# Kernel tuning notes

Hardware: AMD Instinct MI355X
Metric: run time of the kernel (lower is better)

## Reference

```python
import jax, jax.numpy as jnp
import numpy as np

B, S, D, H, DH = 2, 2048, 768, 12, 64
ROT, BASE, WIN = 64, 10000.0, 128
SCALE = float(np.sqrt(DH))  # cfg.attn_scale = sqrt(d_head) = 8.0


def _sin_cos():
    # TransformerLens calculate_sin_cos_rotary, rotary_adjacent_pairs=False
    pos = jnp.arange(S, dtype=jnp.float32)
    freq = BASE ** (jnp.arange(0, ROT, 2, dtype=jnp.float32) / ROT)
    freq = jnp.concatenate([freq, freq])  # 'd -> (2 d)'
    angles = pos[:, None] / freq[None, :]  # [S, ROT]
    return jnp.sin(angles), jnp.cos(angles)


def _rotate_every_two(v):
    n = v.shape[-1] // 2
    return jnp.concatenate([-v[..., n:], v[..., :n]], axis=-1)


def _apply_rotary(x, sin, cos):
    # x: [B, S, H, DH]; rotate first ROT dims, pass rest through
    xr, xp = x[..., :ROT], x[..., ROT:]
    c = cos[None, :, None, :]
    s = sin[None, :, None, :]
    return jnp.concatenate([xr * c + _rotate_every_two(xr) * s, xp], axis=-1)


def setup_inputs() -> dict:
    key = jax.random.key(0)
    ks = jax.random.split(key, 7)
    init = lambda k, shape: jax.random.normal(k, shape, jnp.float32) / np.sqrt(D).astype(np.float32)
    return dict(
        query_input=jax.random.normal(ks[0], (B, S, D), jnp.float32),
        key_input=jax.random.normal(ks[1], (B, S, D), jnp.float32),
        value_input=jax.random.normal(ks[2], (B, S, D), jnp.float32),
        W_Q=init(ks[3], (H, D, DH)),
        W_K=init(ks[4], (H, D, DH)),
        W_V=init(ks[5], (H, D, DH)),
        W_O=init(ks[6], (H, DH, D)),
        b_Q=jnp.zeros((H, DH), jnp.float32),
        b_K=jnp.zeros((H, DH), jnp.float32),
        b_V=jnp.zeros((H, DH), jnp.float32),
        b_O=jnp.zeros((D,), jnp.float32),
    )


def reference(query_input, key_input, value_input, W_Q, W_K, W_V, W_O, b_Q, b_K, b_V, b_O):
    # QKV projections (calculate_qkv_matrices)
    q = jnp.einsum('bpd,hdk->bphk', query_input, W_Q) + b_Q
    k = jnp.einsum('bpd,hdk->bphk', key_input, W_K) + b_K
    v = jnp.einsum('bpd,hdk->bphk', value_input, W_V) + b_V
    # rotary (kv_cache_pos_offset = 0)
    sin, cos = _sin_cos()
    q = _apply_rotary(q, sin, cos)
    k = _apply_rotary(k, sin, cos)
    # attention scores
    scores = jnp.einsum('bqhd,bkhd->bhqk', q, k) / SCALE
    # position_bias defaults to zeros -> no-op
    i = jnp.arange(S)[:, None]
    j = jnp.arange(S)[None, :]
    mask = (j <= i) & (j > i - WIN)
    scores = jnp.where(mask[None, None], scores, -jnp.inf)
    pattern = jax.nn.softmax(scores, axis=-1)
    pattern = jnp.where(jnp.isnan(pattern), 0.0, pattern)
    z = jnp.einsum('bhqk,bkhd->bqhd', pattern, v)  # [B, S, H, DH]
    # output projection: z flattened @ W_O (rearranged) + b_O
    out = z.reshape(B, S, H * DH) @ W_O.reshape(H * DH, D) + b_O
    return out
```

## Files before the change

### kernel.cpp

```cpp
#include <hip/hip_runtime.h>
#include <hip/hip_bf16.h>

#define BB 2
#define SS 2048
#define DD 768
#define HH 12
#define DHH 64
#define WIN 128
#define MM (BB*SS)

typedef __attribute__((ext_vector_type(8))) short bfrag;
typedef __attribute__((ext_vector_type(4))) float f32x4;

#define AS3(p) ((__attribute__((address_space(3))) void*)(p))
#define AS1(p) ((const __attribute__((address_space(1))) void*)(p))

__device__ inline unsigned short f2bf(float f) {
    union { __hip_bfloat16 h; unsigned short u; } cv;
    cv.h = __float2bfloat16(f);
    return cv.u;
}

__device__ inline void stage128(unsigned short* dst, const unsigned short* src,
                                int w4, int l) {
    #pragma unroll
    for (int j = 0; j < 2; j++) {
        int eoff = (w4 * 2 + j) * 512;
        int e = eoff + l * 8;
        int row = e >> 5;
        int k8 = ((e >> 3) & 3) ^ ((row >> 1) & 3);
        __builtin_amdgcn_global_load_lds(AS1(src + (size_t)row * DD + k8 * 8),
                                         AS3(dst + eoff), 16, 0, 0);
    }
}
__device__ inline void stage64(unsigned short* dst, const unsigned short* src,
                               int w4, int l) {
    int eoff = w4 * 512;
    int e = eoff + l * 8;
    int row = e >> 5;
    int k8 = ((e >> 3) & 3) ^ ((row >> 1) & 3);
    __builtin_amdgcn_global_load_lds(AS1(src + (size_t)row * DD + k8 * 8),
                                     AS3(dst + eoff), 16, 0, 0);
}

__global__ __launch_bounds__(256) void pack_kernel(
    const float* __restrict__ Xq, const float* __restrict__ Xk, const float* __restrict__ Xv,
    const float* __restrict__ Wq, const float* __restrict__ Wk, const float* __restrict__ Wv,
    const float* __restrict__ Wo,
    unsigned short* __restrict__ Wt, unsigned short* __restrict__ Wot,
    float2* __restrict__ rope, unsigned short* __restrict__ Xbf)
{
    __shared__ float T[64][65];
    const int bid = blockIdx.x, t = threadIdx.x;
    if (bid < 432) {
        int proj = bid / 144, rem = bid % 144;
        int h = rem / 12, d0 = (rem % 12) * 64;
        const float* src = (proj == 0 ? Wq : (proj == 1 ? Wk : Wv)) + (size_t)h * DD * DHH;
        int row = t >> 2, c0 = (t & 3) * 16;
        const float4* p4 = reinterpret_cast<const float4*>(src + (size_t)(d0 + row) * DHH + c0);
        float4 x0 = p4[0], x1 = p4[1], x2 = p4[2], x3 = p4[3];
        float* tr = &T[row][c0];
        tr[0]=x0.x; tr[1]=x0.y; tr[2]=x0.z; tr[3]=x0.w;
        tr[4]=x1.x; tr[5]=x1.y; tr[6]=x1.z; tr[7]=x1.w;
        tr[8]=x2.x; tr[9]=x2.y; tr[10]=x2.z; tr[11]=x2.w;
        tr[12]=x3.x; tr[13]=x3.y; tr[14]=x3.z; tr[15]=x3.w;
        __syncthreads();
        int dh = t >> 2;
        unsigned short tmp[16];
        #pragma unroll
        for (int j = 0; j < 16; j++) tmp[j] = f2bf(T[c0 + j][dh]);
        unsigned short* dst = Wt + (size_t)proj * DD * DD + (size_t)(h * 64 + dh) * DD + d0 + c0;
        *reinterpret_cast<bfrag*>(dst)     = *reinterpret_cast<bfrag*>(tmp);
        *reinterpret_cast<bfrag*>(dst + 8) = *reinterpret_cast<bfrag*>(tmp + 8);
    } else if (bid < 576) {
        int id2 = bid - 432;
        int k0 = (id2 / 12) * 64, n0 = (id2 % 12) * 64;
        int row = t >> 2, c0 = (t & 3) * 16;
        const float4* p4 = reinterpret_cast<const float4*>(Wo + (size_t)(k0 + row) * DD + n0 + c0);
        float4 x0 = p4[0], x1 = p4[1], x2 = p4[2], x3 = p4[3];
        float* tr = &T[row][c0];
        tr[0]=x0.x; tr[1]=x0.y; tr[2]=x0.z; tr[3]=x0.w;
        tr[4]=x1.x; tr[5]=x1.y; tr[6]=x1.z; tr[7]=x1.w;
        tr[8]=x2.x; tr[9]=x2.y; tr[10]=x2.z; tr[11]=x2.w;
        tr[12]=x3.x; tr[13]=x3.y; tr[14]=x3.z; tr[15]=x3.w;
        __syncthreads();
        int nr = t >> 2;
        unsigned short tmp[16];
        #pragma unroll
        for (int j = 0; j < 16; j++) tmp[j] = f2bf(T[c0 + j][nr]);
        unsigned short* dst = Wot + (size_t)(n0 + nr) * DD + k0 + c0;
        *reinterpret_cast<bfrag*>(dst)     = *reinterpret_cast<bfrag*>(tmp);
        *reinterpret_cast<bfrag*>(dst + 8) = *reinterpret_cast<bfrag*>(tmp + 8);
    } else if (bid < 832) {
        int idx = (bid - 576) * 256 + t;
        int p = idx >> 5, i2 = idx & 31;
        float inv_freq = exp2f(-(float)i2 * (13.287712379549449f / 32.0f));
        float s, c;
        sincosf((float)p * inv_freq, &s, &c);
        rope[idx] = make_float2(s, c);
    } else {
        int i = bid - 832;
        int proj = i / 768;
        size_t off = (size_t)(i % 768) * 4096 + t * 16;
        const float* src = (proj == 0 ? Xq : (proj == 1 ? Xk : Xv)) + off;
        const float4* p4 = reinterpret_cast<const float4*>(src);
        float4 a0 = p4[0], a1 = p4[1], a2 = p4[2], a3 = p4[3];
        unsigned short u[16];
        u[0]=f2bf(a0.x); u[1]=f2bf(a0.y); u[2]=f2bf(a0.z); u[3]=f2bf(a0.w);
        u[4]=f2bf(a1.x); u[5]=f2bf(a1.y); u[6]=f2bf(a1.z); u[7]=f2bf(a1.w);
        u[8]=f2bf(a2.x); u[9]=f2bf(a2.y); u[10]=f2bf(a2.z); u[11]=f2bf(a2.w);
        u[12]=f2bf(a3.x); u[13]=f2bf(a3.y); u[14]=f2bf(a3.z); u[15]=f2bf(a3.w);
        unsigned short* dst = Xbf + (size_t)proj * MM * DD + off;
        *reinterpret_cast<bfrag*>(dst)     = *reinterpret_cast<bfrag*>(u);
        *reinterpret_cast<bfrag*>(dst + 8) = *reinterpret_cast<bfrag*>(u + 8);
    }
}

__global__ __launch_bounds__(256) void qkv_gemm_kernel(
    const unsigned short* __restrict__ Xbf,
    const unsigned short* __restrict__ Wt,
    const float* __restrict__ bq, const float* __restrict__ bk, const float* __restrict__ bv,
    const float2* __restrict__ rope,
    unsigned short* __restrict__ qo, unsigned short* __restrict__ ko, unsigned short* __restrict__ vo)
{
    const int mt0  = blockIdx.x * 128;
    const int n0   = blockIdx.y * 128;
    const int proj = blockIdx.z;
    const unsigned short* X = Xbf + (size_t)proj * MM * DD + (size_t)mt0 * DD;
    const unsigned short* W = Wt + (size_t)proj * DD * DD + (size_t)n0 * DD;
    const float* bias = proj == 0 ? bq : (proj == 1 ? bk : bv);

    __shared__ unsigned short smem[128 * 140];

    const int t = threadIdx.x;
    const int l = t & 63, w4 = t >> 6;
    const int l16 = l & 15, quad = l >> 4;
    const int wr = w4 >> 1, wc = w4 & 1;
    const int swz = (l16 >> 1) & 3;

    f32x4 acc[16] = {};

    stage128(smem,        X, w4, l);
    stage128(smem + 4096, W, w4, l);

    for (int it = 0; it < 24; ++it) {
        unsigned short* Ac = smem + (it & 1) * 8192;
        unsigned short* Bc = Ac + 4096;
        __syncthreads();
        if (it < 23) {
            unsigned short* An = smem + ((it + 1) & 1) * 8192;
            stage128(An,        X + (it + 1) * 32, w4, l);
            stage128(An + 4096, W + (it + 1) * 32, w4, l);
        }
        bfrag af[4], bg[4];
        #pragma unroll
        for (int mi = 0; mi < 4; mi++)
            af[mi] = *reinterpret_cast<const bfrag*>(&Ac[(wr * 64 + mi * 16 + l16) * 32 + ((quad ^ swz) * 8)]);
        #pragma unroll
        for (int ni = 0; ni < 4; ni++)
            bg[ni] = *reinterpret_cast<const bfrag*>(&Bc[(wc * 64 + ni * 16 + l16) * 32 + ((quad ^ swz) * 8)]);
        #pragma unroll
        for (int mi = 0; mi < 4; mi++)
            #pragma unroll
            for (int ni = 0; ni < 4; ni++)
                acc[mi * 4 + ni] = __builtin_amdgcn_mfma_f32_16x16x32_bf16(af[mi], bg[ni], acc[mi * 4 + ni], 0, 0, 0);
    }
    __syncthreads();

    unsigned short* Ct = smem;
    const int b = mt0 >> 11;
    if (proj < 2) {
        #pragma unroll
        for (int ni = 0; ni < 4; ni++) {
            int nloc = wc * 64 + ni * 16 + l16;
            int n = n0 + nloc;
            int dh = n & 63;
            float bv0 = bias[n];
            float bv1 = bias[n ^ 32];
            float sgn = (dh & 32) ? 1.0f : -1.0f;
            const float2* rp = rope + (dh & 31);
            #pragma unroll
            for (int mi = 0; mi < 4; mi++)
                #pragma unroll
                for (int r = 0; r < 4; r++) {
                    int ploc = wr * 64 + mi * 16 + quad * 4 + r;
                    int p = (mt0 + ploc) & (SS - 1);
                    float2 sc = rp[p << 5];
                    float val = acc[mi * 4 + ni][r] + bv0;
                    float pr  = acc[mi * 4 + (ni ^ 2)][r] + bv1;
                    Ct[ploc * 140 + nloc] = f2bf(val * sc.y + sgn * pr * sc.x);
                }
        }
        __syncthreads();
        unsigned short* dst = (proj == 0) ? qo : ko;
        #pragma unroll
        for (int jj = 0; jj < 8; jj++) {
            int id = jj * 256 + t;
            int row = id >> 4, c = (id & 15) * 8;
            int n = n0 + c, h = n >> 6, dh = n & 63;
            int p = (mt0 + row) & (SS - 1);
            bfrag vv = *reinterpret_cast<const bfrag*>(&Ct[row * 140 + c]);
            *reinterpret_cast<bfrag*>(dst + (((size_t)(b * HH + h) * SS + p) << 6) + dh) = vv;
        }
    } else {
        #pragma unroll
        for (int ni = 0; ni < 4; ni++) {
            int nloc = wc * 64 + ni * 16 + l16;
            float bv0 = bias[n0 + nloc];
            #pragma unroll
            for (int mi = 0; mi < 4; mi++)
                #pragma unroll
                for (int r = 0; r < 4; r++) {
                    int ploc = wr * 64 + mi * 16 + quad * 4 + r;
                    Ct[nloc * 140 + ploc] = f2bf(acc[mi * 4 + ni][r] + bv0);
                }
        }
        __syncthreads();
        int p0 = mt0 & (SS - 1);
        #pragma unroll
        for (int jj = 0; jj < 8; jj++) {
            int id = jj * 256 + t;
            int row = id >> 4, c = (id & 15) * 8;
            int n = n0 + row, h = n >> 6, dh = n & 63;
            bfrag vv = *reinterpret_cast<const bfrag*>(&Ct[row * 140 + c]);
            *reinterpret_cast<bfrag*>(vo + (((size_t)(b * HH + h) * DHH + dh) << 11) + p0 + c) = vv;
        }
    }
}

__global__ __launch_bounds__(256) void attn_kernel(
    const unsigned short* __restrict__ q,
    const unsigned short* __restrict__ k,
    const unsigned short* __restrict__ v,
    unsigned short* __restrict__ z)
{
    const int qb = blockIdx.x * 64;
    const int h  = blockIdx.y;
    const int b  = blockIdx.z;
    const int kb = qb - WIN;

    __shared__ unsigned short QK[64 * 72 + 192 * 72];
    __shared__ unsigned short Ps[64 * 200];
    unsigned short* Qs = QK;
    unsigned short* Ks = QK + 64 * 72;
    unsigned short* Vt = QK;

    const int t = threadIdx.x;
    const int w = t >> 6, lane = t & 63;
    const int l16 = lane & 15, quad = lane >> 4;

    const size_t qkbase = ((size_t)(b * HH + h) * SS) * DHH;
    #pragma unroll
    for (int i = 0; i < 2; i++) {
        int chunk = i * 256 + t;
        int row = chunk >> 3, c0 = (chunk & 7) * 8;
        bfrag val = *reinterpret_cast<const bfrag*>(q + qkbase + (size_t)(qb + row) * DHH + c0);
        *reinterpret_cast<bfrag*>(&Qs[row * 72 + c0]) = val;
    }
    #pragma unroll
    for (int i = 0; i < 6; i++) {
        int chunk = i * 256 + t;
        int row = chunk >> 3, c0 = (chunk & 7) * 8;
        int src = kb + row; if (src < 0) src = 0;
        bfrag val = *reinterpret_cast<const bfrag*>(k + qkbase + (size_t)src * DHH + c0);
        *reinterpret_cast<bfrag*>(&Ks[row * 72 + c0]) = val;
    }
    __syncthreads();

    f32x4 sacc[12] = {};
    #pragma unroll
    for (int kk = 0; kk < 64; kk += 32) {
        bfrag a = *reinterpret_cast<const bfrag*>(&Qs[(16 * w + l16) * 72 + kk + quad * 8]);
        #pragma unroll
        for (int mt = 0; mt < 12; mt++) {
            bfrag bf = *reinterpret_cast<const bfrag*>(&Ks[(16 * mt + l16) * 72 + kk + quad * 8]);
            sacc[mt] = __builtin_amdgcn_mfma_f32_16x16x32_bf16(a, bf, sacc[mt], 0, 0, 0);
        }
    }

    float mx[4] = {-3e38f, -3e38f, -3e38f, -3e38f};
    #pragma unroll
    for (int mt = 0; mt < 12; mt++)
        #pragma unroll
        for (int r = 0; r < 4; r++) {
            int row = 16 * w + quad * 4 + r;
            int c = 16 * mt + l16;
            bool valid = (c > row) && (c <= row + WIN) && (kb + c >= 0);
            float s = valid ? sacc[mt][r] * 0.125f : -3e38f;
            sacc[mt][r] = s;
            mx[r] = fmaxf(mx[r], s);
        }
    #pragma unroll
    for (int off = 1; off < 16; off <<= 1)
        #pragma unroll
        for (int r = 0; r < 4; r++) mx[r] = fmaxf(mx[r], __shfl_xor(mx[r], off, 64));
    float sum[4] = {0.f, 0.f, 0.f, 0.f};
    #pragma unroll
    for (int mt = 0; mt < 12; mt++)
        #pragma unroll
        for (int r = 0; r < 4; r++) {
            float p = __expf(sacc[mt][r] - mx[r]);
            sacc[mt][r] = p;
            sum[r] += p;
        }
    #pragma unroll
    for (int off = 1; off < 16; off <<= 1)
        #pragma unroll
        for (int r = 0; r < 4; r++) sum[r] += __shfl_xor(sum[r], off, 64);
    float inv[4];
    #pragma unroll
    for (int r = 0; r < 4; r++) inv[r] = 1.0f / sum[r];

    #pragma unroll
    for (int mt = 0; mt < 12; mt++)
        #pragma unroll
        for (int r = 0; r < 4; r++)
            Ps[(16 * w + quad * 4 + r) * 200 + 16 * mt + l16] = f2bf(sacc[mt][r] * inv[r]);
    __syncthreads();

    const size_t vbase = ((size_t)(b * HH + h) * DHH) * SS;
    if (kb >= 0) {
        #pragma unroll
        for (int i = 0; i < 6; i++) {
            int chunk = i * 256 + t;
            int d = chunk / 24, c0 = (chunk % 24) * 8;
            bfrag val = *reinterpret_cast<const bfrag*>(v + vbase + (size_t)d * SS + kb + c0);
            *reinterpret_cast<bfrag*>(&Vt[d * 200 + c0]) = val;
        }
    } else {
        for (int i = 0; i < 6; i++) {
            int chunk = i * 256 + t;
            int d = chunk / 24, c0 = (chunk % 24) * 8;
            unsigned short tmp[8];
            for (int j2 = 0; j2 < 8; j2++) {
                int src = kb + c0 + j2; if (src < 0) src = 0;
                tmp[j2] = v[vbase + (size_t)d * SS + src];
            }
            for (int j2 = 0; j2 < 8; j2++) Vt[d * 200 + c0 + j2] = tmp[j2];
        }
    }
    __syncthreads();

    f32x4 zacc[4] = {};
    #pragma unroll
    for (int c0 = 0; c0 < 192; c0 += 32) {
        bfrag a = *reinterpret_cast<const bfrag*>(&Ps[(16 * w + l16) * 200 + c0 + quad * 8]);
        #pragma unroll
        for (int nt = 0; nt < 4; nt++) {
            bfrag bf = *reinterpret_cast<const bfrag*>(&Vt[(16 * nt + l16) * 200 + c0 + quad * 8]);
            zacc[nt] = __builtin_amdgcn_mfma_f32_16x16x32_bf16(a, bf, zacc[nt], 0, 0, 0);
        }
    }
    #pragma unroll
    for (int nt = 0; nt < 4; nt++)
        #pragma unroll
        for (int r = 0; r < 4; r++) {
            int row = 16 * w + quad * 4 + r;
            int d = 16 * nt + l16;
            z[((size_t)(b * SS + qb + row)) * (HH * DHH) + h * DHH + d] = f2bf(zacc[nt][r]);
        }
}

__global__ __launch_bounds__(256) void out_gemm_kernel(
    const unsigned short* __restrict__ Z,
    const unsigned short* __restrict__ Wot,
    const float* __restrict__ bo,
    float* __restrict__ out)
{
    const int mt0 = blockIdx.x * 64;
    const int n0  = blockIdx.y * 128;
    const unsigned short* A = Z + (size_t)mt0 * DD;
    const unsigned short* Bw = Wot + (size_t)n0 * DD;

    __shared__ unsigned short smem[12288];

    const int t = threadIdx.x;
    const int l = t & 63, w4 = t >> 6;
    const int l16 = l & 15, quad = l >> 4;
    const int swz = (l16 >> 1) & 3;

    f32x4 acc[8] = {};

    stage64 (smem,        A,  w4, l);
    stage128(smem + 2048, Bw, w4, l);

    for (int it = 0; it < 24; ++it) {
        unsigned short* Ac = smem + (it & 1) * 6144;
        unsigned short* Bc = Ac + 2048;
        __syncthreads();
        if (it < 23) {
            unsigned short* An = smem + ((it + 1) & 1) * 6144;
            stage64 (An,        A  + (it + 1) * 32, w4, l);
            stage128(An + 2048, Bw + (it + 1) * 32, w4, l);
        }
        bfrag af[4], bg[2];
        #pragma unroll
        for (int mi = 0; mi < 4; mi++)
            af[mi] = *reinterpret_cast<const bfrag*>(&Ac[(mi * 16 + l16) * 32 + ((quad ^ swz) * 8)]);
        #pragma unroll
        for (int ni = 0; ni < 2; ni++)
            bg[ni] = *reinterpret_cast<const bfrag*>(&Bc[(w4 * 32 + ni * 16 + l16) * 32 + ((quad ^ swz) * 8)]);
        #pragma unroll
        for (int mi = 0; mi < 4; mi++)
            #pragma unroll
            for (int ni = 0; ni < 2; ni++)
                acc[mi * 2 + ni] = __builtin_amdgcn_mfma_f32_16x16x32_bf16(af[mi], bg[ni], acc[mi * 2 + ni], 0, 0, 0);
    }

    #pragma unroll
    for (int ni = 0; ni < 2; ni++) {
        int n = n0 + w4 * 32 + ni * 16 + l16;
        float bv0 = bo[n];
        #pragma unroll
        for (int mi = 0; mi < 4; mi++)
            #pragma unroll
            for (int r = 0; r < 4; r++) {
                int m = mt0 + mi * 16 + quad * 4 + r;
                out[(size_t)m * DD + n] = acc[mi * 2 + ni][r] + bv0;
            }
    }
}

extern "C" void kernel_launch(void* const* d_in, const int* in_sizes, int n_in,
                              void* d_out, int out_size, void* d_ws, size_t ws_size,
                              hipStream_t stream) {
    const float* Xq = (const float*)d_in[0];
    const float* Xk = (const float*)d_in[1];
    const float* Xv = (const float*)d_in[2];
    const float* Wq = (const float*)d_in[3];
    const float* Wk = (const float*)d_in[4];
    const float* Wv = (const float*)d_in[5];
    const float* Wo = (const float*)d_in[6];
    const float* bq = (const float*)d_in[7];
    const float* bk = (const float*)d_in[8];
    const float* bv = (const float*)d_in[9];
    const float* bo = (const float*)d_in[10];
    float* out = (float*)d_out;

    const size_t seg = (size_t)BB * HH * SS * DHH;
    unsigned short* q   = (unsigned short*)d_ws;
    unsigned short* k   = q + seg;
    unsigned short* v   = k + seg;
    unsigned short* z   = v + seg;
    unsigned short* Wt  = z + seg;
    unsigned short* Wot = Wt + (size_t)3 * DD * DD;
    float2* rope = (float2*)(Wot + (size_t)DD * DD);
    unsigned short* Xbf = (unsigned short*)(rope + 2048 * 32);

    pack_kernel<<<dim3(3136), 256, 0, stream>>>(Xq, Xk, Xv, Wq, Wk, Wv, Wo, Wt, Wot, rope, Xbf);
    qkv_gemm_kernel<<<dim3(MM / 128, DD / 128, 3), 256, 0, stream>>>(
        Xbf, Wt, bq, bk, bv, rope, q, k, v);
    attn_kernel<<<dim3(SS / 64, HH, BB), 256, 0, stream>>>(q, k, v, z);
    out_gemm_kernel<<<dim3(MM / 64, DD / 128), 256, 0, stream>>>(z, Wot, bo, out);
}
```

Before: 169.1 us.

## Shrink QKV GEMM M-tile to 64 and restructure attention operand staging

The QKV GEMM moves from 128x128 to 64x128 tiles, doubling the grid and cutting shared memory so more blocks can be resident. The attention kernel now stages K into swizzled LDS with async global-to-LDS loads, keeps Q and V fragments in registers loaded straight from global memory, and reuses the K buffer for the probabilities. It computes Z transposed so each lane stores a 4-wide packed vector. This removes the separate V staging pass and one barrier, at the cost of more register pressure. For the first query block kb is negative, so the V and K loads read before the start of the buffer instead of clamping, and correctness there depends on masking alone.

```diff
diff --git a/kernel.cpp b/kernel.cpp
--- a/kernel.cpp
+++ b/kernel.cpp
@@ -11,6 +11,7 @@
 
 typedef __attribute__((ext_vector_type(8))) short bfrag;
 typedef __attribute__((ext_vector_type(4))) float f32x4;
+typedef __attribute__((ext_vector_type(4))) short s16x4;
 
 #define AS3(p) ((__attribute__((address_space(3))) void*)(p))
 #define AS1(p) ((const __attribute__((address_space(1))) void*)(p))
@@ -19,28 +20,6 @@
     union { __hip_bfloat16 h; unsigned short u; } cv;
     cv.h = __float2bfloat16(f);
     return cv.u;
-}
-
-__device__ inline void stage128(unsigned short* dst, const unsigned short* src,
-                                int w4, int l) {
-    #pragma unroll
-    for (int j = 0; j < 2; j++) {
-        int eoff = (w4 * 2 + j) * 512;
-        int e = eoff + l * 8;
-        int row = e >> 5;
-        int k8 = ((e >> 3) & 3) ^ ((row >> 1) & 3);
-        __builtin_amdgcn_global_load_lds(AS1(src + (size_t)row * DD + k8 * 8),
-                                         AS3(dst + eoff), 16, 0, 0);
-    }
-}
-__device__ inline void stage64(unsigned short* dst, const unsigned short* src,
-                               int w4, int l) {
-    int eoff = w4 * 512;
-    int e = eoff + l * 8;
-    int row = e >> 5;
-    int k8 = ((e >> 3) & 3) ^ ((row >> 1) & 3);
-    __builtin_amdgcn_global_load_lds(AS1(src + (size_t)row * DD + k8 * 8),
-                                     AS3(dst + eoff), 16, 0, 0);
 }
 
 __global__ __launch_bounds__(256) void pack_kernel(
@@ -123,14 +102,14 @@
     const float2* __restrict__ rope,
     unsigned short* __restrict__ qo, unsigned short* __restrict__ ko, unsigned short* __restrict__ vo)
 {
-    const int mt0  = blockIdx.x * 128;
+    const int mt0  = blockIdx.x * 64;
     const int n0   = blockIdx.y * 128;
     const int proj = blockIdx.z;
     const unsigned short* X = Xbf + (size_t)proj * MM * DD + (size_t)mt0 * DD;
     const unsigned short* W = Wt + (size_t)proj * DD * DD + (size_t)n0 * DD;
     const float* bias = proj == 0 ? bq : (proj == 1 ? bk : bv);
 
-    __shared__ unsigned short smem[128 * 140];
+    __shared__ unsigned short smem[12288];
 
     const int t = threadIdx.x;
     const int l = t & 63, w4 = t >> 6;
@@ -138,29 +117,48 @@
     const int wr = w4 >> 1, wc = w4 & 1;
     const int swz = (l16 >> 1) & 3;
 
-    f32x4 acc[16] = {};
-
-    stage128(smem,        X, w4, l);
-    stage128(smem + 4096, W, w4, l);
+    f32x4 acc[8] = {};
+
+    #define STAGE_QKV(bufp, k0)                                                   \
+        _Pragma("unroll")                                                         \
+        for (int j = 0; j < 3; j++) {                                             \
+            int g = w4 * 3 + j;                                                   \
+            if (g < 4) {                                                          \
+                int e = g * 512 + l * 8;                                          \
+                int row = e >> 5;                                                 \
+                int k8 = ((e >> 3) & 3) ^ ((row >> 1) & 3);                       \
+                __builtin_amdgcn_global_load_lds(                                 \
+                    AS1(X + (size_t)row * DD + (k0) + k8 * 8),                    \
+                    AS3((bufp) + g * 512), 16, 0, 0);                             \
+            } else {                                                              \
+                int g2 = g - 4;                                                   \
+                int e = g2 * 512 + l * 8;                                         \
+                int row = e >> 5;                                                 \
+                int k8 = ((e >> 3) & 3) ^ ((row >> 1) & 3);                       \
+                __builtin_amdgcn_global_load_lds(                                 \
+                    AS1(W + (size_t)row * DD + (k0) + k8 * 8),                    \
+                    AS3((bufp) + 2048 + g2 * 512), 16, 0, 0);                     \
+            }                                                                     \
+        }
+
+    STAGE_QKV(smem, 0)
 
     for (int it = 0; it < 24; ++it) {
-        unsigned short* Ac = smem + (it & 1) * 8192;
-        unsigned short* Bc = Ac + 4096;
+        unsigned short* cur = smem + (it & 1) * 6144;
         __syncthreads();
         if (it < 23) {
-            unsigned short* An = smem + ((it + 1) & 1) * 8192;
-            stage128(An,        X + (it + 1) * 32, w4, l);
-            stage128(An + 4096, W + (it + 1) * 32, w4, l);
-        }
-        bfrag af[4], bg[4];
-        #pragma unroll
-        for (int mi = 0; mi < 4; mi++)
-            af[mi] = *reinterpret_cast<const bfrag*>(&Ac[(wr * 64 + mi * 16 + l16) * 32 + ((quad ^ swz) * 8)]);
+            unsigned short* nxt = smem + ((it + 1) & 1) * 6144;
+            STAGE_QKV(nxt, (it + 1) * 32)
+        }
+        bfrag af[2], bg[4];
+        #pragma unroll
+        for (int mi = 0; mi < 2; mi++)
+            af[mi] = *reinterpret_cast<const bfrag*>(&cur[(wr * 32 + mi * 16 + l16) * 32 + ((quad ^ swz) * 8)]);
         #pragma unroll
         for (int ni = 0; ni < 4; ni++)
-            bg[ni] = *reinterpret_cast<const bfrag*>(&Bc[(wc * 64 + ni * 16 + l16) * 32 + ((quad ^ swz) * 8)]);
-        #pragma unroll
-        for (int mi = 0; mi < 4; mi++)
+            bg[ni] = *reinterpret_cast<const bfrag*>(&cur[2048 + (wc * 64 + ni * 16 + l16) * 32 + ((quad ^ swz) * 8)]);
+        #pragma unroll
+        for (int mi = 0; mi < 2; mi++)
             #pragma unroll
             for (int ni = 0; ni < 4; ni++)
                 acc[mi * 4 + ni] = __builtin_amdgcn_mfma_f32_16x16x32_bf16(af[mi], bg[ni], acc[mi * 4 + ni], 0, 0, 0);
@@ -169,6 +167,7 @@
 
     unsigned short* Ct = smem;
     const int b = mt0 >> 11;
+    const int p0 = mt0 & (SS - 1);
     if (proj < 2) {
         #pragma unroll
         for (int ni = 0; ni < 4; ni++) {
@@ -180,12 +179,11 @@
             float sgn = (dh & 32) ? 1.0f : -1.0f;
             const float2* rp = rope + (dh & 31);
             #pragma unroll
-            for (int mi = 0; mi < 4; mi++)
+            for (int mi = 0; mi < 2; mi++)
                 #pragma unroll
                 for (int r = 0; r < 4; r++) {
-                    int ploc = wr * 64 + mi * 16 + quad * 4 + r;
-                    int p = (mt0 + ploc) & (SS - 1);
-                    float2 sc = rp[p << 5];
+                    int ploc = wr * 32 + mi * 16 + quad * 4 + r;
+                    float2 sc = rp[(p0 + ploc) << 5];
                     float val = acc[mi * 4 + ni][r] + bv0;
                     float pr  = acc[mi * 4 + (ni ^ 2)][r] + bv1;
                     Ct[ploc * 140 + nloc] = f2bf(val * sc.y + sgn * pr * sc.x);
@@ -194,13 +192,12 @@
         __syncthreads();
         unsigned short* dst = (proj == 0) ? qo : ko;
         #pragma unroll
-        for (int jj = 0; jj < 8; jj++) {
+        for (int jj = 0; jj < 4; jj++) {
             int id = jj * 256 + t;
             int row = id >> 4, c = (id & 15) * 8;
             int n = n0 + c, h = n >> 6, dh = n & 63;
-            int p = (mt0 + row) & (SS - 1);
             bfrag vv = *reinterpret_cast<const bfrag*>(&Ct[row * 140 + c]);
-            *reinterpret_cast<bfrag*>(dst + (((size_t)(b * HH + h) * SS + p) << 6) + dh) = vv;
+            *reinterpret_cast<bfrag*>(dst + (((size_t)(b * HH + h) * SS + p0 + row) << 6) + dh) = vv;
         }
     } else {
         #pragma unroll
@@ -208,24 +205,24 @@
             int nloc = wc * 64 + ni * 16 + l16;
             float bv0 = bias[n0 + nloc];
             #pragma unroll
-            for (int mi = 0; mi < 4; mi++)
+            for (int mi = 0; mi < 2; mi++)
                 #pragma unroll
                 for (int r = 0; r < 4; r++) {
-                    int ploc = wr * 64 + mi * 16 + quad * 4 + r;
-                    Ct[nloc * 140 + ploc] = f2bf(acc[mi * 4 + ni][r] + bv0);
+                    int ploc = wr * 32 + mi * 16 + quad * 4 + r;
+                    Ct[nloc * 72 + ploc] = f2bf(acc[mi * 4 + ni][r] + bv0);
                 }
         }
         __syncthreads();
-        int p0 = mt0 & (SS - 1);
-        #pragma unroll
-        for (int jj = 0; jj < 8; jj++) {
+        #pragma unroll
+        for (int jj = 0; jj < 4; jj++) {
             int id = jj * 256 + t;
-            int row = id >> 4, c = (id & 15) * 8;
+            int row = id >> 3, c = (id & 7) * 8;
             int n = n0 + row, h = n >> 6, dh = n & 63;
-            bfrag vv = *reinterpret_cast<const bfrag*>(&Ct[row * 140 + c]);
+            bfrag vv = *reinterpret_cast<const bfrag*>(&Ct[row * 72 + c]);
             *reinterpret_cast<bfrag*>(vo + (((size_t)(b * HH + h) * DHH + dh) << 11) + p0 + c) = vv;
         }
     }
+    #undef STAGE_QKV
 }
 
 __global__ __launch_bounds__(256) void attn_kernel(
@@ -239,51 +236,69 @@
     const int b  = blockIdx.z;
     const int kb = qb - WIN;
 
-    __shared__ unsigned short QK[64 * 72 + 192 * 72];
-    __shared__ unsigned short Ps[64 * 200];
-    unsigned short* Qs = QK;
-    unsigned short* Ks = QK + 64 * 72;
-    unsigned short* Vt = QK;
+    __shared__ unsigned short sA[12800];
 
     const int t = threadIdx.x;
-    const int w = t >> 6, lane = t & 63;
-    const int l16 = lane & 15, quad = lane >> 4;
-
-    const size_t qkbase = ((size_t)(b * HH + h) * SS) * DHH;
-    #pragma unroll
-    for (int i = 0; i < 2; i++) {
-        int chunk = i * 256 + t;
-        int row = chunk >> 3, c0 = (chunk & 7) * 8;
-        bfrag val = *reinterpret_cast<const bfrag*>(q + qkbase + (size_t)(qb + row) * DHH + c0);
-        *reinterpret_cast<bfrag*>(&Qs[row * 72 + c0]) = val;
-    }
-    #pragma unroll
-    for (int i = 0; i < 6; i++) {
-        int chunk = i * 256 + t;
-        int row = chunk >> 3, c0 = (chunk & 7) * 8;
-        int src = kb + row; if (src < 0) src = 0;
-        bfrag val = *reinterpret_cast<const bfrag*>(k + qkbase + (size_t)src * DHH + c0);
-        *reinterpret_cast<bfrag*>(&Ks[row * 72 + c0]) = val;
-    }
+    const int w4 = t >> 6, l = t & 63;
+    const int l16 = l & 15, quad = l >> 4;
+    const int swz = (l16 >> 1) & 3;
+
+    const size_t qkbase = (size_t)(b * HH + h) * SS * DHH;
+    const unsigned short* kp = (k + qkbase) + (ptrdiff_t)kb * DHH;
+    const unsigned short* vp = (v + (size_t)(b * HH + h) * DHH * SS) + (ptrdiff_t)kb;
+
+    #pragma unroll
+    for (int j = 0; j < 6; j++) {
+        int g = w4 * 6 + j;
+        int panel = g >> 2, sub = g & 3;
+        int rg = panel >> 1, kpart = panel & 1;
+        int e = sub * 512 + l * 8;
+        int row = e >> 5;
+        int k8 = ((e >> 3) & 3) ^ ((row >> 1) & 3);
+        __builtin_amdgcn_global_load_lds(
+            AS1(kp + (size_t)(rg * 64 + row) * DHH + kpart * 32 + k8 * 8),
+            AS3(sA + panel * 2048 + sub * 512), 16, 0, 0);
+    }
+    bfrag qf[2];
+    #pragma unroll
+    for (int kk = 0; kk < 2; kk++)
+        qf[kk] = *reinterpret_cast<const bfrag*>(
+            q + qkbase + (size_t)(qb + 16 * w4 + l16) * DHH + kk * 32 + quad * 8);
+    bfrag vfA[12];
+    #pragma unroll
+    for (int ci = 0; ci < 3; ci++)
+        #pragma unroll
+        for (int mt = 0; mt < 4; mt++)
+            vfA[ci * 4 + mt] = *reinterpret_cast<const bfrag*>(
+                vp + (size_t)(16 * mt + l16) * SS + ci * 32 + quad * 8);
+
     __syncthreads();
 
     f32x4 sacc[12] = {};
     #pragma unroll
-    for (int kk = 0; kk < 64; kk += 32) {
-        bfrag a = *reinterpret_cast<const bfrag*>(&Qs[(16 * w + l16) * 72 + kk + quad * 8]);
+    for (int kk = 0; kk < 2; kk++)
         #pragma unroll
         for (int mt = 0; mt < 12; mt++) {
-            bfrag bf = *reinterpret_cast<const bfrag*>(&Ks[(16 * mt + l16) * 72 + kk + quad * 8]);
-            sacc[mt] = __builtin_amdgcn_mfma_f32_16x16x32_bf16(a, bf, sacc[mt], 0, 0, 0);
-        }
-    }
+            int kr = 16 * mt + l16;
+            bfrag bf = *reinterpret_cast<const bfrag*>(
+                &sA[(((kr >> 6) * 2 + kk) * 2048) + (kr & 63) * 32 + ((quad ^ swz) * 8)]);
+            sacc[mt] = __builtin_amdgcn_mfma_f32_16x16x32_bf16(qf[kk], bf, sacc[mt], 0, 0, 0);
+        }
+
+    bfrag vfB[12];
+    #pragma unroll
+    for (int ci = 0; ci < 3; ci++)
+        #pragma unroll
+        for (int mt = 0; mt < 4; mt++)
+            vfB[ci * 4 + mt] = *reinterpret_cast<const bfrag*>(
+                vp + (size_t)(16 * mt + l16) * SS + (ci + 3) * 32 + quad * 8);
 
     float mx[4] = {-3e38f, -3e38f, -3e38f, -3e38f};
     #pragma unroll
     for (int mt = 0; mt < 12; mt++)
         #pragma unroll
         for (int r = 0; r < 4; r++) {
-            int row = 16 * w + quad * 4 + r;
+            int row = 16 * w4 + quad * 4 + r;
             int c = 16 * mt + l16;
             bool valid = (c > row) && (c <= row + WIN) && (kb + c >= 0);
             float s = valid ? sacc[mt][r] * 0.125f : -3e38f;
@@ -311,54 +326,58 @@
     #pragma unroll
     for (int r = 0; r < 4; r++) inv[r] = 1.0f / sum[r];
 
+    __syncthreads();
+
+    unsigned short* Ps = sA;
     #pragma unroll
     for (int mt = 0; mt < 12; mt++)
         #pragma unroll
         for (int r = 0; r < 4; r++)
-            Ps[(16 * w + quad * 4 + r) * 200 + 16 * mt + l16] = f2bf(sacc[mt][r] * inv[r]);
-    __syncthreads();
-
-    const size_t vbase = ((size_t)(b * HH + h) * DHH) * SS;
-    if (kb >= 0) {
-        #pragma unroll
-        for (int i = 0; i < 6; i++) {
-            int chunk = i * 256 + t;
-            int d = chunk / 24, c0 = (chunk % 24) * 8;
-            bfrag val = *reinterpret_cast<const bfrag*>(v + vbase + (size_t)d * SS + kb + c0);
-            *reinterpret_cast<bfrag*>(&Vt[d * 200 + c0]) = val;
-        }
-    } else {
-        for (int i = 0; i < 6; i++) {
-            int chunk = i * 256 + t;
-            int d = chunk / 24, c0 = (chunk % 24) * 8;
-            unsigned short tmp[8];
-            for (int j2 = 0; j2 < 8; j2++) {
-                int src = kb + c0 + j2; if (src < 0) src = 0;
-                tmp[j2] = v[vbase + (size_t)d * SS + src];
-            }
-            for (int j2 = 0; j2 < 8; j2++) Vt[d * 200 + c0 + j2] = tmp[j2];
-        }
-    }
-    __syncthreads();
+            Ps[(16 * w4 + quad * 4 + r) * 200 + 16 * mt + l16] = f2bf(sacc[mt][r] * inv[r]);
 
     f32x4 zacc[4] = {};
     #pragma unroll
-    for (int c0 = 0; c0 < 192; c0 += 32) {
-        bfrag a = *reinterpret_cast<const bfrag*>(&Ps[(16 * w + l16) * 200 + c0 + quad * 8]);
-        #pragma unroll
-        for (int nt = 0; nt < 4; nt++) {
-            bfrag bf = *reinterpret_cast<const bfrag*>(&Vt[(16 * nt + l16) * 200 + c0 + quad * 8]);
-            zacc[nt] = __builtin_amdgcn_mfma_f32_16x16x32_bf16(a, bf, zacc[nt], 0, 0, 0);
-        }
-    }
-    #pragma unroll
-    for (int nt = 0; nt < 4; nt++)
-        #pragma unroll
-        for (int r = 0; r < 4; r++) {
-            int row = 16 * w + quad * 4 + r;
-            int d = 16 * nt + l16;
-            z[((size_t)(b * SS + qb + row)) * (HH * DHH) + h * DHH + d] = f2bf(zacc[nt][r]);
-        }
+    for (int ci = 0; ci < 6; ci++) {
+        bfrag pb = *reinterpret_cast<const bfrag*>(
+            &Ps[(16 * w4 + l16) * 200 + ci * 32 + quad * 8]);
+        #pragma unroll
+        for (int mt = 0; mt < 4; mt++) {
+            bfrag va = (ci < 3) ? vfA[ci * 4 + mt] : vfB[(ci - 3) * 4 + mt];
+            zacc[mt] = __builtin_amdgcn_mfma_f32_16x16x32_bf16(va, pb, zacc[mt], 0, 0, 0);
+        }
+    }
+    size_t zrow = ((size_t)(b * SS + qb + 16 * w4 + l16)) * (HH * DHH) + h * DHH;
+    #pragma unroll
+    for (int mt = 0; mt < 4; mt++) {
+        s16x4 pk;
+        pk[0] = (short)f2bf(zacc[mt][0]);
+        pk[1] = (short)f2bf(zacc[mt][1]);
+        pk[2] = (short)f2bf(zacc[mt][2]);
+        pk[3] = (short)f2bf(zacc[mt][3]);
+        *reinterpret_cast<s16x4*>(z + zrow + 16 * mt + quad * 4) = pk;
+    }
+}
+
+__device__ inline void stage128(unsigned short* dst, const unsigned short* src,
+                                int w4, int l) {
+    #pragma unroll
+    for (int j = 0; j < 2; j++) {
+        int eoff = (w4 * 2 + j) * 512;
+        int e = eoff + l * 8;
+        int row = e >> 5;
+        int k8 = ((e >> 3) & 3) ^ ((row >> 1) & 3);
+        __builtin_amdgcn_global_load_lds(AS1(src + (size_t)row * DD + k8 * 8),
+                                         AS3(dst + eoff), 16, 0, 0);
+    }
+}
+__device__ inline void stage64(unsigned short* dst, const unsigned short* src,
+                               int w4, int l) {
+    int eoff = w4 * 512;
+    int e = eoff + l * 8;
+    int row = e >> 5;
+    int k8 = ((e >> 3) & 3) ^ ((row >> 1) & 3);
+    __builtin_amdgcn_global_load_lds(AS1(src + (size_t)row * DD + k8 * 8),
+                                     AS3(dst + eoff), 16, 0, 0);
 }
 
 __global__ __launch_bounds__(256) void out_gemm_kernel(
@@ -448,7 +467,7 @@
     unsigned short* Xbf = (unsigned short*)(rope + 2048 * 32);
 
     pack_kernel<<<dim3(3136), 256, 0, stream>>>(Xq, Xk, Xv, Wq, Wk, Wv, Wo, Wt, Wot, rope, Xbf);
-    qkv_gemm_kernel<<<dim3(MM / 128, DD / 128, 3), 256, 0, stream>>>(
+    qkv_gemm_kernel<<<dim3(MM / 64, DD / 128, 3), 256, 0, stream>>>(
         Xbf, Wt, bq, bk, bv, rope, q, k, v);
     attn_kernel<<<dim3(SS / 64, HH, BB), 256, 0, stream>>>(q, k, v, z);
     out_gemm_kernel<<<dim3(MM / 64, DD / 128), 256, 0, stream>>>(z, Wot, bo, out);
```

After: 169.0 us. No clear change (-0.1%).
